# Kernel optimization log

Hardware: AMD Instinct MI355X
Metric: run time of the kernel (lower is better)

## Reference

```python
import math
import jax, jax.numpy as jnp
import numpy as np

B, T, C, H, D = 2, 2048, 1024, 16, 64


def make_rope_cache(seq_len, head_dim, base=10000.0):
    half = head_dim // 2
    inv_freq = 1.0 / (base ** (np.arange(0, half, dtype=np.float32) / half))
    t = np.arange(seq_len, dtype=np.float32)
    freqs = np.outer(t, inv_freq)  # (T, D/2)
    cache = np.stack([np.cos(freqs), np.sin(freqs)], axis=1)  # (T, 2, D/2)
    return jnp.asarray(cache, dtype=jnp.float32)


def setup_inputs() -> dict:
    key = jax.random.key(0)
    ks = jax.random.split(key, 6)
    s = 1.0 / math.sqrt(C)
    return {
        "x": jax.random.normal(ks[0], (B, T, C), dtype=jnp.float32),
        "rope_cache": make_rope_cache(T, D),
        "Wq": jax.random.normal(ks[1], (C, C), dtype=jnp.float32) * s,
        "Wk": jax.random.normal(ks[2], (C, C), dtype=jnp.float32) * s,
        "Wv": jax.random.normal(ks[3], (C, C), dtype=jnp.float32) * s,
        "Wo": jax.random.normal(ks[4], (C, C), dtype=jnp.float32) * s,
        "mask": jnp.ones((B, T), dtype=jnp.bool_),
    }


def apply_rope(x, rope_cache):
    # x: (B, T, H, D); rope_cache: (T, 2, D//2)
    seq_len = x.shape[1]
    cos = rope_cache[:seq_len, 0, :][None, :, None, :]
    sin = rope_cache[:seq_len, 1, :][None, :, None, :]
    half = x.shape[-1] // 2
    x1, x2 = x[..., :half], x[..., half:]
    return jnp.concatenate([x1 * cos - x2 * sin, x1 * sin + x2 * cos], axis=-1)


def reference(x, rope_cache, Wq, Wk, Wv, Wo, mask):
    b, t, c = x.shape
    q = (x @ Wq).reshape(b, t, H, D)
    k = (x @ Wk).reshape(b, t, H, D)
    v = (x @ Wv).reshape(b, t, H, D)
    q = apply_rope(q, rope_cache).transpose(0, 2, 1, 3)  # (B,H,T,D)
    k = apply_rope(k, rope_cache).transpose(0, 2, 1, 3)
    v = v.transpose(0, 2, 1, 3)
    scale = 1.0 / math.sqrt(D)
    attn = jnp.einsum('bhid,bhjd->bhij', q, k) * scale  # (B,H,T,T)
    causal = jnp.tril(jnp.ones((t, t), dtype=jnp.bool_))
    attn = jnp.where(causal[None, None, :, :], attn, -1e9)
    attn = jnp.where(mask[:, None, None, :], attn, -1e9)
    attn = jax.nn.softmax(attn, axis=-1)
    out = jnp.einsum('bhij,bhjd->bhid', attn, v)
    out = out.transpose(0, 2, 1, 3).reshape(b, t, c)
    return out @ Wo
```

## Files before the change

kernel.cpp:

```cpp
#include <hip/hip_runtime.h>


typedef short s16x8 __attribute__((ext_vector_type(8)));
typedef __bf16 bf16x8 __attribute__((ext_vector_type(8)));
typedef float f32x4 __attribute__((ext_vector_type(4)));
typedef float f32x16 __attribute__((ext_vector_type(16)));
typedef unsigned u32x4 __attribute__((ext_vector_type(4)));
typedef unsigned u32x2 __attribute__((ext_vector_type(2)));

__device__ __forceinline__ short f2bf(float f) {
  unsigned u = __builtin_bit_cast(unsigned, f);
  u += 0x7fffu + ((u >> 16) & 1u);
  return (short)(u >> 16);
}

__device__ __forceinline__ unsigned cvtpk(float lo, float hi) {
  unsigned r;
  asm("v_cvt_pk_bf16_f32 %0, %1, %2" : "=v"(r) : "v"(lo), "v"(hi));
  return r;
}

__device__ __forceinline__ f32x4 mfma16(s16x8 a, s16x8 b, f32x4 c) {
  return __builtin_amdgcn_mfma_f32_16x16x32_bf16(
      __builtin_bit_cast(bf16x8, a), __builtin_bit_cast(bf16x8, b), c, 0, 0, 0);
}

__device__ __forceinline__ f32x16 mfma32(s16x8 a, s16x8 b, f32x16 c) {
  return __builtin_amdgcn_mfma_f32_32x32x16_bf16(
      __builtin_bit_cast(bf16x8, a), __builtin_bit_cast(bf16x8, b), c, 0, 0, 0);
}

__device__ __forceinline__ void gload16(const void* g, void* l) {
  __builtin_amdgcn_global_load_lds(
      (__attribute__((address_space(1))) void*)(void*)g,
      (__attribute__((address_space(3))) void*)l, 16, 0, 0);
}

__global__ void cvt_fused_kernel(const float* __restrict__ xin,
                                 const float* __restrict__ Wq, const float* __restrict__ Wk,
                                 const float* __restrict__ Wv, const float* __restrict__ Wo,
                                 short* __restrict__ xb, short* __restrict__ wt) {
  __shared__ float t32[32][33];
  int bid = blockIdx.x;
  int tid = threadIdx.x;
  if (bid < 2048) {
    int i = bid * 256 + tid;
    const float4* p = (const float4*)xin + (size_t)i * 2;
    float4 a = p[0], b = p[1];
    s16x8 o;
    o[0] = f2bf(a.x); o[1] = f2bf(a.y); o[2] = f2bf(a.z); o[3] = f2bf(a.w);
    o[4] = f2bf(b.x); o[5] = f2bf(b.y); o[6] = f2bf(b.z); o[7] = f2bf(b.w);
    ((s16x8*)xb)[i] = o;
  } else {
    int b = bid - 2048;
    int z = b >> 10;
    int rem = b & 1023;
    int n0 = (rem & 31) * 32, k0 = (rem >> 5) * 32;
    const float* W = (z == 0) ? Wq : (z == 1) ? Wk : (z == 2) ? Wv : Wo;
    short* o = wt + (size_t)z * 1024 * 1024;
    int tx = tid & 31, ty = tid >> 5;
#pragma unroll
    for (int i = 0; i < 4; ++i) t32[ty + 8 * i][tx] = W[(size_t)(k0 + ty + 8 * i) * 1024 + n0 + tx];
    __syncthreads();
#pragma unroll
    for (int i = 0; i < 4; ++i) o[(size_t)(n0 + ty + 8 * i) * 1024 + k0 + tx] = f2bf(t32[tx][ty + 8 * i]);
  }
}

__global__ __launch_bounds__(256) void qkv_gemm_kernel(
    const short* __restrict__ xb, const short* __restrict__ wt,
    const float* __restrict__ rope,
    short* __restrict__ Qo, short* __restrict__ Ko, short* __restrict__ Vt) {
  __shared__ short S[12288];
  short* As = S;
  short* Bs = S + 8192;
  int bid = blockIdx.x;
  int mt = bid & 31;
  int ntile = bid >> 5;
  int mat = ntile >> 4;
  int h = ntile & 15;
  int tid = threadIdx.x, lane = tid & 63, w = tid >> 6;
  int rloc = lane & 15, lgrp = lane >> 4;
  int e3 = rloc & 7;

  const char* Agb0 = (const char*)(xb + (size_t)mt * 128 * 1024);
  const char* Bgb0 = (const char*)(wt + (size_t)mat * 1024 * 1024 + (size_t)h * 64 * 1024);

  f32x4 acc[2][4];
#pragma unroll
  for (int m = 0; m < 2; ++m)
#pragma unroll
    for (int n = 0; n < 4; ++n) acc[m][n] = (f32x4){0.f, 0.f, 0.f, 0.f};

  for (int kt = 0; kt < 16; ++kt) {
    __syncthreads();
    const char* Ag = Agb0 + kt * 128;
    const char* Bg = Bgb0 + kt * 128;
#pragma unroll
    for (int rr = 0; rr < 4; ++rr) {
      int lin = rr * 4096 + tid * 16;
      int row = lin >> 7;
      int ch = (lin >> 4) & 7;
      int srcoff = (row << 11) + ((ch ^ (row & 7)) << 4);
      gload16(Ag + srcoff, (char*)As + lin);
    }
#pragma unroll
    for (int rr = 0; rr < 2; ++rr) {
      int lin = rr * 4096 + tid * 16;
      int row = lin >> 7;
      int ch = (lin >> 4) & 7;
      int srcoff = (row << 11) + ((ch ^ (row & 7)) << 4);
      gload16(Bg + srcoff, (char*)Bs + lin);
    }
    __syncthreads();
#pragma unroll
    for (int kk = 0; kk < 2; ++kk) {
      s16x8 a[2], b[4];
#pragma unroll
      for (int m = 0; m < 2; ++m)
        a[m] = *(const s16x8*)&As[(w * 32 + m * 16 + rloc) * 64 + (((kk * 4 + lgrp) ^ e3) << 3)];
#pragma unroll
      for (int n = 0; n < 4; ++n)
        b[n] = *(const s16x8*)&Bs[(n * 16 + rloc) * 64 + (((kk * 4 + lgrp) ^ e3) << 3)];
      __builtin_amdgcn_s_setprio(1);
#pragma unroll
      for (int m = 0; m < 2; ++m)
#pragma unroll
        for (int n = 0; n < 4; ++n) acc[m][n] = mfma16(a[m], b[n], acc[m][n]);
      __builtin_amdgcn_s_setprio(0);
    }
  }

  if (mat < 2) {
    bool isK = (mat == 1);
    float csf = isK ? 1.0f : (0.125f * 1.44269504088896340736f);
    short* dst = (mat == 0) ? Qo : Ko;
#pragma unroll
    for (int m = 0; m < 2; ++m) {
#pragma unroll
      for (int j = 0; j < 4; ++j) {
        int rowg = mt * 128 + w * 32 + m * 16 + lgrp * 4 + j;
        int bI = rowg >> 11, t = rowg & 2047;
        short* hb = dst + (((size_t)(bI * 16 + h)) * 2048 + t) * 64;
#pragma unroll
        for (int n = 0; n < 2; ++n) {
          int d = n * 16 + rloc;
          float cs = rope[t * 64 + d] * csf;
          float sn = rope[t * 64 + 32 + d] * csf;
          float a0 = acc[m][n][j], b0 = acc[m][n + 2][j];
          int d2 = d + 32;
          int a1 = isK ? ((((d >> 3) ^ (t & 7)) << 3) | (d & 7)) : d;
          int a2 = isK ? ((((d2 >> 3) ^ (t & 7)) << 3) | (d & 7)) : d2;
          hb[a1] = f2bf(a0 * cs - b0 * sn);
          hb[a2] = f2bf(a0 * sn + b0 * cs);
        }
      }
    }
  } else {
    __syncthreads();
    short* T = S;
#pragma unroll
    for (int m = 0; m < 2; ++m)
#pragma unroll
      for (int j = 0; j < 4; ++j) {
        int t_in = w * 32 + m * 16 + lgrp * 4 + j;
#pragma unroll
        for (int n = 0; n < 4; ++n) {
          int d = n * 16 + rloc;
          T[t_in * 66 + d] = f2bf(acc[m][n][j]);
        }
      }
    __syncthreads();
    int d = tid & 63;
    int th = tid >> 6;
    int t0g = mt * 128;
    int bI = t0g >> 11;
    short* vrow = Vt + (((size_t)(bI * 16 + h)) * 64 + d) * 2048 + (t0g & 2047);
#pragma unroll
    for (int c = 0; c < 4; ++c) {
      int tw0 = th * 32 + c * 8;
      s16x8 pk;
#pragma unroll
      for (int i = 0; i < 8; ++i) pk[i] = T[(tw0 + i) * 66 + d];
      int gr = (((tw0 >> 3) & 15) ^ (d & 15)) << 3;
      *(s16x8*)(vrow + gr) = pk;
    }
  }
}

__global__ __launch_bounds__(256, 2) void attn_kernel(
    const short* __restrict__ Q, const short* __restrict__ K,
    const short* __restrict__ Vt, short* __restrict__ O) {
  __shared__ short Ks[3][64 * 64];
  __shared__ short Vs[3][64 * 64];
  int tid = threadIdx.x;
  int lane = tid & 63;
  int w = tid >> 6;
  int bh = blockIdx.x;
  int qb = 15 - (int)blockIdx.y;
  int qv = lane & 31, h = lane >> 5;
  int q0 = qb * 128 + w * 32;
  int tq = q0 + qv;

  const short* Qg = Q + ((size_t)bh * 2048 + q0) * 64;
  s16x8 qf[4];
#pragma unroll
  for (int kq = 0; kq < 4; ++kq)
    qf[kq] = *(const s16x8*)(Qg + qv * 64 + kq * 16 + h * 8);

  const char* KgB = (const char*)(K + (size_t)bh * 2048 * 64);
  const char* VgB = (const char*)(Vt + (size_t)bh * 64 * 2048);

  f32x16 l_acc;
  f32x16 ot0, ot1;
#pragma unroll
  for (int r = 0; r < 16; ++r) { ot0[r] = 0.f; ot1[r] = 0.f; l_acc[r] = 0.f; }

  int nkv = 2 * qb + 2;

  auto STAGE = [&](int slot, int kt) {
    int k0 = kt << 6;
    const char* Kg = KgB + (size_t)k0 * 128;
    char* kd = (char*)&Ks[slot][0];
    char* vd = (char*)&Vs[slot][0];
    gload16(Kg + tid * 16, kd + tid * 16);
    gload16(Kg + 4096 + tid * 16, kd + 4096 + tid * 16);
    size_t vwin = (size_t)((k0 & ~127) * 2);
    int kpar = (k0 >> 6) & 1;
    {
      int lin = tid * 16;
      int d = lin >> 7, col = lin & 127;
      int ho = (((d >> 3) & 1) ^ kpar) << 7;
      gload16(VgB + (size_t)d * 4096 + vwin + ho + col, vd + lin);
    }
    {
      int lin = 4096 + tid * 16;
      int d = lin >> 7, col = lin & 127;
      int ho = (((d >> 3) & 1) ^ kpar) << 7;
      gload16(VgB + (size_t)d * 4096 + vwin + ho + col, vd + lin);
    }
  };

  STAGE(0, 0);
  STAGE(1, 1);

  for (int kt = 0; kt < nkv; ++kt) {
    int b = kt % 3;
    int k0 = kt << 6;
    if (kt + 2 < nkv) STAGE((kt + 2) % 3, kt + 2);
    if (kt + 2 < nkv)      asm volatile("s_waitcnt vmcnt(8)" ::: "memory");
    else if (kt + 1 < nkv) asm volatile("s_waitcnt vmcnt(4)" ::: "memory");
    else                   asm volatile("s_waitcnt vmcnt(0)" ::: "memory");
    __builtin_amdgcn_s_barrier();

    bool act = (k0 <= q0 + 31);
    if (act) {
      f32x16 s[2];
#pragma unroll
      for (int n = 0; n < 2; ++n)
#pragma unroll
        for (int r = 0; r < 16; ++r) s[n][r] = 0.f;
      __builtin_amdgcn_s_setprio(1);
#pragma unroll
      for (int n = 0; n < 2; ++n) {
        int r = n * 32 + qv;
#pragma unroll
        for (int kq = 0; kq < 4; ++kq) {
          s16x8 ka = *(const s16x8*)&Ks[b][r * 64 + (((2 * kq + h) ^ (r & 7)) << 3)];
          s[n] = mfma32(ka, qf[kq], s[n]);
        }
      }
      __builtin_amdgcn_s_setprio(0);
      if (k0 + 63 > q0) {
#pragma unroll
        for (int n = 0; n < 2; ++n)
#pragma unroll
          for (int r = 0; r < 16; ++r) {
            int tk = k0 + n * 32 + (r & 3) + ((r >> 2) << 3) + h * 4;
            if (tk > tq) s[n][r] = -3.0e38f;
          }
      }
#pragma unroll
      for (int n = 0; n < 2; ++n)
#pragma unroll
        for (int r = 0; r < 16; ++r)
          s[n][r] = exp2f(s[n][r]);
      l_acc += s[0] + s[1];

#pragma unroll
      for (int n = 0; n < 2; ++n) {
        unsigned dA[4], dB[4];
#pragma unroll
        for (int m = 0; m < 4; ++m) {
          dA[m] = cvtpk(s[n][4 * m], s[n][4 * m + 1]);
          dB[m] = cvtpk(s[n][4 * m + 2], s[n][4 * m + 3]);
        }
#pragma unroll
        for (int c = 0; c < 2; ++c) {
          u32x4 fv;
#if __has_builtin(__builtin_amdgcn_permlane32_swap)
          u32x2 pa = __builtin_amdgcn_permlane32_swap(dA[2 * c], dA[2 * c + 1], false, false);
          u32x2 pb = __builtin_amdgcn_permlane32_swap(dB[2 * c], dB[2 * c + 1], false, false);
          fv[0] = pa[0]; fv[1] = pb[0]; fv[2] = pa[1]; fv[3] = pb[1];
#else
          unsigned sendA = h ? dA[2 * c] : dA[2 * c + 1];
          unsigned sendB = h ? dB[2 * c] : dB[2 * c + 1];
          unsigned ownA  = h ? dA[2 * c + 1] : dA[2 * c];
          unsigned ownB  = h ? dB[2 * c + 1] : dB[2 * c];
          unsigned rA = (unsigned)__shfl_xor((int)sendA, 32);
          unsigned rB = (unsigned)__shfl_xor((int)sendB, 32);
          fv[0] = h ? rA : ownA;
          fv[1] = h ? rB : ownB;
          fv[2] = h ? ownA : rA;
          fv[3] = h ? ownB : rB;
#endif
          s16x8 pf = __builtin_bit_cast(s16x8, fv);
          int kk = 2 * n + c;
          int slot = ((2 * kk + h) ^ (qv & 7)) << 3;
          s16x8 va0 = *(const s16x8*)&Vs[b][qv * 64 + slot];
          s16x8 va1 = *(const s16x8*)&Vs[b][(32 + qv) * 64 + slot];
          __builtin_amdgcn_s_setprio(1);
          ot0 = mfma32(va0, pf, ot0);
          ot1 = mfma32(va1, pf, ot1);
          __builtin_amdgcn_s_setprio(0);
        }
      }
    }
    __builtin_amdgcn_s_barrier();
  }

  float r8[8];
#pragma unroll
  for (int i = 0; i < 8; ++i) r8[i] = l_acc[i] + l_acc[i + 8];
#pragma unroll
  for (int off = 4; off > 0; off >>= 1)
#pragma unroll
    for (int i = 0; i < 4; ++i)
      if (i < off) r8[i] += r8[i + off];
  float l_run = r8[0];
  float l_tot = l_run + __shfl_xor(l_run, 32);
  float inv = 1.0f / l_tot;
  int bI = bh >> 4, h16 = bh & 15;
  short* Og = O + ((size_t)bI * 2048 + tq) * 1024 + h16 * 64;
#pragma unroll
  for (int r = 0; r < 16; r += 2) {
    int d = (r & 3) + ((r >> 2) << 3) + h * 4;
    *(unsigned*)(Og + d)      = cvtpk(ot0[r] * inv, ot0[r + 1] * inv);
    *(unsigned*)(Og + 32 + d) = cvtpk(ot1[r] * inv, ot1[r + 1] * inv);
  }
}

__global__ __launch_bounds__(256) void out_gemm_kernel(
    const short* __restrict__ Ob, const short* __restrict__ wto,
    float* __restrict__ out) {
  __shared__ short As[128 * 64];
  __shared__ short Bs[64 * 64];
  int bid = blockIdx.x;
  int mt = bid & 31, nt = bid >> 5;
  int tid = threadIdx.x, lane = tid & 63, w = tid >> 6;
  int rloc = lane & 15, lgrp = lane >> 4;
  int e3 = rloc & 7;

  const char* Agb0 = (const char*)(Ob + (size_t)mt * 128 * 1024);
  const char* Bgb0 = (const char*)(wto + (size_t)nt * 64 * 1024);

  f32x4 acc[2][4];
#pragma unroll
  for (int m = 0; m < 2; ++m)
#pragma unroll
    for (int n = 0; n < 4; ++n) acc[m][n] = (f32x4){0.f, 0.f, 0.f, 0.f};

  for (int kt = 0; kt < 16; ++kt) {
    __syncthreads();
    const char* Ag = Agb0 + kt * 128;
    const char* Bg = Bgb0 + kt * 128;
#pragma unroll
    for (int rr = 0; rr < 4; ++rr) {
      int lin = rr * 4096 + w * 1024 + lane * 16;
      int row = lin >> 7;
      int ch = (lin >> 4) & 7;
      int srcoff = (row << 11) + ((ch ^ (row & 7)) << 4);
      gload16(Ag + srcoff, (char*)As + lin);
    }
#pragma unroll
    for (int rr = 0; rr < 2; ++rr) {
      int lin = rr * 4096 + w * 1024 + lane * 16;
      int row = lin >> 7;
      int ch = (lin >> 4) & 7;
      int srcoff = (row << 11) + ((ch ^ (row & 7)) << 4);
      gload16(Bg + srcoff, (char*)Bs + lin);
    }
    __syncthreads();
#pragma unroll
    for (int kk = 0; kk < 2; ++kk) {
      s16x8 a[2], b[4];
#pragma unroll
      for (int m = 0; m < 2; ++m)
        a[m] = *(const s16x8*)&As[(w * 32 + m * 16 + rloc) * 64 + (((kk * 4 + lgrp) ^ e3) << 3)];
#pragma unroll
      for (int n = 0; n < 4; ++n)
        b[n] = *(const s16x8*)&Bs[(n * 16 + rloc) * 64 + (((kk * 4 + lgrp) ^ e3) << 3)];
#pragma unroll
      for (int m = 0; m < 2; ++m)
#pragma unroll
        for (int n = 0; n < 4; ++n) acc[m][n] = mfma16(a[m], b[n], acc[m][n]);
    }
  }

#pragma unroll
  for (int m = 0; m < 2; ++m)
#pragma unroll
    for (int j = 0; j < 4; ++j) {
      int rowg = mt * 128 + w * 32 + m * 16 + lgrp * 4 + j;
#pragma unroll
      for (int n = 0; n < 4; ++n) {
        int colg = nt * 64 + n * 16 + rloc;
        out[(size_t)rowg * 1024 + colg] = acc[m][n][j];
      }
    }
}

extern "C" void kernel_launch(void* const* d_in, const int* in_sizes, int n_in,
                              void* d_out, int out_size, void* d_ws, size_t ws_size,
                              hipStream_t stream) {
  const float* x    = (const float*)d_in[0];
  const float* rope = (const float*)d_in[1];
  const float* Wq   = (const float*)d_in[2];
  const float* Wk   = (const float*)d_in[3];
  const float* Wv   = (const float*)d_in[4];
  const float* Wo   = (const float*)d_in[5];

  char* ws = (char*)d_ws;
  short* xb  = (short*)(ws);
  short* wt  = (short*)(ws + ((size_t)8  << 20));
  short* Qb  = (short*)(ws + ((size_t)16 << 20));
  short* Kb  = (short*)(ws + ((size_t)24 << 20));
  short* Vtb = (short*)(ws + ((size_t)32 << 20));
  short* Ob  = (short*)(ws + ((size_t)40 << 20));

  cvt_fused_kernel<<<6144, 256, 0, stream>>>(x, Wq, Wk, Wv, Wo, xb, wt);
  qkv_gemm_kernel<<<1536, 256, 0, stream>>>(xb, wt, rope, Qb, Kb, Vtb);
  attn_kernel<<<dim3(32, 16), 256, 0, stream>>>(Qb, Kb, Vtb, Ob);
  out_gemm_kernel<<<512, 256, 0, stream>>>(Ob, wt + (size_t)3 * 1024 * 1024, (float*)d_out);
}
```

Measured before the change: 110.0 us.

## Double-buffer QKV GEMM LDS tiles and remap block IDs for XCD locality

The QKV projection GEMM now keeps two shared-memory buffers and issues the global-to-LDS loads for the next K-tile before computing on the current one. A partial vmcnt wait plus raw barriers replaces the two full __syncthreads per iteration, so load latency can overlap MFMA work. Both the QKV and output GEMMs also remap block IDs so that consecutive tiles sharing an A row-block land on the same XCD, aiming to improve L2 reuse. The cost is double the LDS footprint, which may lower occupancy, and a dependence on exact vmcnt counting for correctness.

```diff
diff --git a/kernel.cpp b/kernel.cpp
--- a/kernel.cpp
+++ b/kernel.cpp
@@ -71,12 +71,12 @@
     const short* __restrict__ xb, const short* __restrict__ wt,
     const float* __restrict__ rope,
     short* __restrict__ Qo, short* __restrict__ Ko, short* __restrict__ Vt) {
-  __shared__ short S[12288];
-  short* As = S;
-  short* Bs = S + 8192;
+  __shared__ short As[2][128 * 64];
+  __shared__ short Bs[2][64 * 64];
   int bid = blockIdx.x;
-  int mt = bid & 31;
-  int ntile = bid >> 5;
+  int wgid = (bid & 7) * 192 + (bid >> 3);
+  int mt = wgid / 48;
+  int ntile = wgid % 48;
   int mat = ntile >> 4;
   int h = ntile & 15;
   int tid = threadIdx.x, lane = tid & 63, w = tid >> 6;
@@ -92,17 +92,18 @@
 #pragma unroll
     for (int n = 0; n < 4; ++n) acc[m][n] = (f32x4){0.f, 0.f, 0.f, 0.f};
 
-  for (int kt = 0; kt < 16; ++kt) {
-    __syncthreads();
+  auto STAGE = [&](int buf, int kt) {
     const char* Ag = Agb0 + kt * 128;
     const char* Bg = Bgb0 + kt * 128;
+    char* ad = (char*)&As[buf][0];
+    char* bd = (char*)&Bs[buf][0];
 #pragma unroll
     for (int rr = 0; rr < 4; ++rr) {
       int lin = rr * 4096 + tid * 16;
       int row = lin >> 7;
       int ch = (lin >> 4) & 7;
       int srcoff = (row << 11) + ((ch ^ (row & 7)) << 4);
-      gload16(Ag + srcoff, (char*)As + lin);
+      gload16(Ag + srcoff, ad + lin);
     }
 #pragma unroll
     for (int rr = 0; rr < 2; ++rr) {
@@ -110,18 +111,29 @@
       int row = lin >> 7;
       int ch = (lin >> 4) & 7;
       int srcoff = (row << 11) + ((ch ^ (row & 7)) << 4);
-      gload16(Bg + srcoff, (char*)Bs + lin);
-    }
-    __syncthreads();
+      gload16(Bg + srcoff, bd + lin);
+    }
+  };
+
+  STAGE(0, 0);
+  for (int kt = 0; kt < 16; ++kt) {
+    int cur = kt & 1;
+    if (kt + 1 < 16) {
+      STAGE(cur ^ 1, kt + 1);
+      asm volatile("s_waitcnt vmcnt(6)" ::: "memory");
+    } else {
+      asm volatile("s_waitcnt vmcnt(0)" ::: "memory");
+    }
+    __builtin_amdgcn_s_barrier();
 #pragma unroll
     for (int kk = 0; kk < 2; ++kk) {
       s16x8 a[2], b[4];
 #pragma unroll
       for (int m = 0; m < 2; ++m)
-        a[m] = *(const s16x8*)&As[(w * 32 + m * 16 + rloc) * 64 + (((kk * 4 + lgrp) ^ e3) << 3)];
+        a[m] = *(const s16x8*)&As[cur][(w * 32 + m * 16 + rloc) * 64 + (((kk * 4 + lgrp) ^ e3) << 3)];
 #pragma unroll
       for (int n = 0; n < 4; ++n)
-        b[n] = *(const s16x8*)&Bs[(n * 16 + rloc) * 64 + (((kk * 4 + lgrp) ^ e3) << 3)];
+        b[n] = *(const s16x8*)&Bs[cur][(n * 16 + rloc) * 64 + (((kk * 4 + lgrp) ^ e3) << 3)];
       __builtin_amdgcn_s_setprio(1);
 #pragma unroll
       for (int m = 0; m < 2; ++m)
@@ -129,6 +141,7 @@
         for (int n = 0; n < 4; ++n) acc[m][n] = mfma16(a[m], b[n], acc[m][n]);
       __builtin_amdgcn_s_setprio(0);
     }
+    __builtin_amdgcn_s_barrier();
   }
 
   if (mat < 2) {
@@ -158,7 +171,7 @@
     }
   } else {
     __syncthreads();
-    short* T = S;
+    short* T = &As[0][0];
 #pragma unroll
     for (int m = 0; m < 2; ++m)
 #pragma unroll
@@ -356,7 +369,8 @@
   __shared__ short As[128 * 64];
   __shared__ short Bs[64 * 64];
   int bid = blockIdx.x;
-  int mt = bid & 31, nt = bid >> 5;
+  int wgid = (bid & 7) * 64 + (bid >> 3);
+  int mt = wgid >> 4, nt = wgid & 15;
   int tid = threadIdx.x, lane = tid & 63, w = tid >> 6;
   int rloc = lane & 15, lgrp = lane >> 4;
   int e3 = rloc & 7;
```

Result: no change. 110.2 us (+0.2%).
